# Kernel optimization log

Measured on AMD Instinct MI355X. Metric: run time of the kernel, lower is better.

The kernel has to match this reference:

```python
import jax, jax.numpy as jnp
import numpy as np

N, E = 50000, 800000
IN, HID, OUT = 256, 128, 64


def setup_inputs() -> dict:
    key = jax.random.key(0)
    ks = jax.random.split(key, 8)
    x = jax.random.normal(ks[0], (N, IN), dtype=jnp.float32)
    edge_index = jax.random.randint(ks[1], (2, E), 0, N, dtype=jnp.int64)
    # PyG GCNConv: Linear weight [out, in] (glorot-ish), bias [out] (zeros init; use small randn for a nontrivial baseline)
    W1 = jax.random.normal(ks[2], (HID, IN), dtype=jnp.float32) / np.sqrt(IN)
    b1 = jax.random.normal(ks[3], (HID,), dtype=jnp.float32) * 0.01
    Wmu = jax.random.normal(ks[4], (OUT, HID), dtype=jnp.float32) / np.sqrt(HID)
    bmu = jax.random.normal(ks[5], (OUT,), dtype=jnp.float32) * 0.01
    Wlv = jax.random.normal(ks[6], (OUT, HID), dtype=jnp.float32) / np.sqrt(HID)
    blv = jax.random.normal(ks[7], (OUT,), dtype=jnp.float32) * 0.01
    return {"x": x, "edge_index": edge_index, "W1": W1, "b1": b1,
            "Wmu": Wmu, "bmu": bmu, "Wlv": Wlv, "blv": blv}


def reference(x, edge_index, W1, b1, Wmu, bmu, Wlv, blv):
    n = x.shape[0]
    loop = jnp.arange(n, dtype=edge_index.dtype)
    src = jnp.concatenate([edge_index[0], loop])  # [E+N]
    dst = jnp.concatenate([edge_index[1], loop])
    # symmetric normalization with self-loops: deg computed on destinations
    deg = jax.ops.segment_sum(jnp.ones_like(dst, dtype=x.dtype), dst, num_segments=n)
    dis = jax.lax.rsqrt(deg)  # deg >= 1 due to self-loops
    norm = dis[src] * dis[dst]  # [E+N]

    def gcn(h, W, b):
        hw = h @ W.T                                   # [N, out]
        msg = hw[src] * norm[:, None]                  # [E+N, out] gather + scale
        return jax.ops.segment_sum(msg, dst, num_segments=n) + b

    h = jax.nn.relu(gcn(x, W1, b1))
    # dropout(p=0.5) is identity in eval mode
    return (gcn(h, Wmu, bmu), gcn(h, Wlv, blv))
```

## Files before the change

### kernel.cpp

```cpp
#include <hip/hip_runtime.h>

#define N_NODES 50000
#define N_EDGES 800000
#define DIN 256
#define DHID 128
#define DOUT 64
#define NB_SCAN 49
#define SENT N_NODES

typedef __attribute__((ext_vector_type(8))) short short8;
typedef __attribute__((ext_vector_type(4))) float f32x4;

static __device__ __forceinline__ short f2bf(float f) {
    union { float f; unsigned u; } v; v.f = f;
    unsigned r = v.u + 0x7FFFu + ((v.u >> 16) & 1u);
    return (short)(r >> 16);
}
static __device__ __forceinline__ float bflo(unsigned p) {
    union { unsigned u; float f; } v; v.u = p << 16; return v.f;
}
static __device__ __forceinline__ float bfhi(unsigned p) {
    union { unsigned u; float f; } v; v.u = p & 0xFFFF0000u; return v.f;
}


__global__ void count_kernel(const int* __restrict__ ei, int* __restrict__ cnt,
                             int* __restrict__ loc) {
    int stride = gridDim.x * blockDim.x;
    for (int e = blockIdx.x * blockDim.x + threadIdx.x; e < N_EDGES; e += stride) {
        loc[e] = atomicAdd(&cnt[ei[N_EDGES + e]], 1);
    }
}

__global__ __launch_bounds__(1024) void bsum_kernel(const int* __restrict__ cnt,
                                                    int* __restrict__ bsum) {
    __shared__ int ws[16];
    int tid = threadIdx.x, i = blockIdx.x * 1024 + tid;
    int v = (i < N_NODES) ? cnt[i] : 0;
    v = (v + 7) & ~7;
    #pragma unroll
    for (int off = 32; off >= 1; off >>= 1) v += __shfl_xor(v, off);
    if ((tid & 63) == 0) ws[tid >> 6] = v;
    __syncthreads();
    if (tid == 0) {
        int s = 0;
        #pragma unroll
        for (int w = 0; w < 16; ++w) s += ws[w];
        bsum[blockIdx.x] = s;
    }
}

__global__ void bscan_kernel(const int* __restrict__ bsum, int* __restrict__ bo,
                             int* __restrict__ rowptr) {
    int l = threadIdx.x;
    int v = (l < NB_SCAN) ? bsum[l] : 0;
    int x = v;
    #pragma unroll
    for (int off = 1; off < 64; off <<= 1) {
        int y = __shfl_up(x, off);
        if (l >= off) x += y;
    }
    if (l < NB_SCAN) bo[l] = x - v;
    if (l == 63) rowptr[N_NODES] = x;
}

__global__ __launch_bounds__(1024) void scan_apply_kernel(const int* __restrict__ cnt,
        const int* __restrict__ bo, int* __restrict__ rowptr,
        float* __restrict__ dis, int* __restrict__ col) {
    __shared__ int wsum[16];
    int tid = threadIdx.x, i = blockIdx.x * 1024 + tid;
    int lane = tid & 63, wid = tid >> 6;
    int v = (i < N_NODES) ? cnt[i] : 0;
    int p = (v + 7) & ~7;
    int x = p;
    #pragma unroll
    for (int off = 1; off < 64; off <<= 1) {
        int y = __shfl_up(x, off);
        if (lane >= off) x += y;
    }
    if (lane == 63) wsum[wid] = x;
    __syncthreads();
    if (tid == 0) {
        int s = 0;
        #pragma unroll
        for (int w = 0; w < 16; ++w) { int t = wsum[w]; wsum[w] = s; s += t; }
    }
    __syncthreads();
    int excl = bo[blockIdx.x] + wsum[wid] + (x - p);
    if (i < N_NODES) {
        rowptr[i] = excl;
        dis[i] = rsqrtf((float)(v + 1));
        for (int q = v; q < p; ++q) col[excl + q] = SENT;
    }
}

__global__ void fill_kernel(const int* __restrict__ ei, const int* __restrict__ loc,
                            const int* __restrict__ rowptr, int* __restrict__ col) {
    int stride = gridDim.x * blockDim.x;
    for (int e = blockIdx.x * blockDim.x + threadIdx.x; e < N_EDGES; e += stride) {
        int s = ei[e];
        int d = ei[N_EDGES + e];
        col[rowptr[d] + loc[e]] = s;
    }
}


__global__ void wprep_kernel(const float* __restrict__ W1, const float* __restrict__ Wmu,
                             const float* __restrict__ Wlv, short* __restrict__ W1b,
                             short* __restrict__ Wctb) {
    int tid = blockIdx.x * blockDim.x + threadIdx.x;
    if (tid < DHID * DIN) {
        W1b[tid] = f2bf(W1[tid]);
    } else if (tid < DHID * DIN + 2 * DOUT * DHID) {
        int t = tid - DHID * DIN;
        Wctb[t] = f2bf((t < DOUT * DHID) ? Wmu[t] : Wlv[t - DOUT * DHID]);
    }
}


__global__ __launch_bounds__(256) void gemm1_mfma_kernel(const float* __restrict__ x,
        const short* __restrict__ W1b, const float* __restrict__ dis,
        short* __restrict__ u1b) {
    const int lane = threadIdx.x & 63, w = threadIdx.x >> 6;
    const int l15 = lane & 15, kg = lane >> 4;
    const int nb = blockIdx.x * 64;
    const int r0 = nb + w * 16 + l15;
    const bool valid = r0 < N_NODES;
    const float* xrow = x + (size_t)r0 * DIN;

    float4 f0[8], f1[8];
    #pragma unroll
    for (int ks = 0; ks < 8; ++ks) {
        const int k0 = ks * 32 + kg * 8;
        if (valid) {
            f0[ks] = *(const float4*)(xrow + k0);
            f1[ks] = *(const float4*)(xrow + k0 + 4);
        } else {
            f0[ks] = float4{0.f, 0.f, 0.f, 0.f};
            f1[ks] = float4{0.f, 0.f, 0.f, 0.f};
        }
    }
    short8 a[8];
    #pragma unroll
    for (int ks = 0; ks < 8; ++ks) {
        a[ks][0] = f2bf(f0[ks].x); a[ks][1] = f2bf(f0[ks].y);
        a[ks][2] = f2bf(f0[ks].z); a[ks][3] = f2bf(f0[ks].w);
        a[ks][4] = f2bf(f1[ks].x); a[ks][5] = f2bf(f1[ks].y);
        a[ks][6] = f2bf(f1[ks].z); a[ks][7] = f2bf(f1[ks].w);
    }

    f32x4 acc[8] = {};
    #pragma unroll
    for (int ks = 0; ks < 8; ++ks) {
        const int k0 = ks * 32 + kg * 8;
        #pragma unroll
        for (int c = 0; c < 8; ++c) {
            short8 b = *(const short8*)(W1b + (size_t)(c * 16 + l15) * DIN + k0);
            acc[c] = __builtin_amdgcn_mfma_f32_16x16x32_bf16(a[ks], b, acc[c], 0, 0, 0);
        }
    }

    const int rb = nb + w * 16 + kg * 4;
    float dv[4];
    #pragma unroll
    for (int e = 0; e < 4; ++e) dv[e] = (rb + e < N_NODES) ? dis[rb + e] : 0.f;
    #pragma unroll
    for (int c = 0; c < 8; ++c) {
        #pragma unroll
        for (int e = 0; e < 4; ++e) {
            int r = rb + e;
            if (r < N_NODES)
                u1b[(size_t)r * DHID + c * 16 + l15] = f2bf(acc[c][e] * dv[e]);
        }
    }
}


template <bool LAYER1>
__global__ __launch_bounds__(256) void pull_kernel(const int* __restrict__ rowptr,
        const int* __restrict__ col, const short* __restrict__ uin,
        const float* __restrict__ dis, const float* __restrict__ b1,
        unsigned* __restrict__ uout) {
    const int wid = threadIdx.x >> 6, lane = threadIdx.x & 63;
    const int i = blockIdx.x * 4 + wid;
    if (i >= N_NODES) return;
    const int beg = rowptr[i], end = rowptr[i + 1];
    const unsigned* __restrict__ up = (const unsigned*)uin;
    float ax = 0.f, ay = 0.f;
    for (int base = beg; base < end; base += 64) {
        const int rem = end - base;
        const int m = rem < 64 ? rem : 64;
        int cv = (lane < m) ? col[base + lane] : SENT;
        for (int t = 0; t < m; t += 8) {
            int c0 = __shfl(cv, t);
            int c1 = __shfl(cv, t + 1);
            int c2 = __shfl(cv, t + 2);
            int c3 = __shfl(cv, t + 3);
            int c4 = __shfl(cv, t + 4);
            int c5 = __shfl(cv, t + 5);
            int c6 = __shfl(cv, t + 6);
            int c7 = __shfl(cv, t + 7);
            unsigned v0 = up[(size_t)c0 * 64 + lane];
            unsigned v1 = up[(size_t)c1 * 64 + lane];
            unsigned v2 = up[(size_t)c2 * 64 + lane];
            unsigned v3 = up[(size_t)c3 * 64 + lane];
            unsigned v4 = up[(size_t)c4 * 64 + lane];
            unsigned v5 = up[(size_t)c5 * 64 + lane];
            unsigned v6 = up[(size_t)c6 * 64 + lane];
            unsigned v7 = up[(size_t)c7 * 64 + lane];
            ax += bflo(v0); ay += bfhi(v0);
            ax += bflo(v1); ay += bfhi(v1);
            ax += bflo(v2); ay += bfhi(v2);
            ax += bflo(v3); ay += bfhi(v3);
            ax += bflo(v4); ay += bfhi(v4);
            ax += bflo(v5); ay += bfhi(v5);
            ax += bflo(v6); ay += bfhi(v6);
            ax += bflo(v7); ay += bfhi(v7);
        }
    }
    const float di = dis[i];
    const unsigned sv = up[(size_t)i * 64 + lane];
    float tx = di * (ax + bflo(sv));
    float ty = di * (ay + bfhi(sv));
    if (LAYER1) {
        float2 b = *(const float2*)(b1 + lane * 2);
        tx = fmaxf(tx + b.x, 0.f) * di;
        ty = fmaxf(ty + b.y, 0.f) * di;
    }
    unsigned o = ((unsigned)(unsigned short)f2bf(tx)) |
                 (((unsigned)(unsigned short)f2bf(ty)) << 16);
    uout[(size_t)i * 64 + lane] = o;
}


__global__ __launch_bounds__(256) void gemm2_mfma_kernel(const short* __restrict__ a2b,
        const short* __restrict__ Wctb, const float* __restrict__ bmu,
        const float* __restrict__ blv, float* __restrict__ out) {
    const int lane = threadIdx.x & 63, w = threadIdx.x >> 6;
    const int l15 = lane & 15, kg = lane >> 4;
    const int nb = blockIdx.x * 64;
    const int r0 = nb + w * 16 + l15;
    const bool valid = r0 < N_NODES;
    const short* arow = a2b + (size_t)r0 * DHID;

    f32x4 acc[8] = {};
    #pragma unroll
    for (int ks = 0; ks < 4; ++ks) {
        const int k0 = ks * 32 + kg * 8;
        short8 a = valid ? *(const short8*)(arow + k0)
                         : short8{0, 0, 0, 0, 0, 0, 0, 0};
        #pragma unroll
        for (int c = 0; c < 8; ++c) {
            short8 b = *(const short8*)(Wctb + (size_t)(c * 16 + l15) * DHID + k0);
            acc[c] = __builtin_amdgcn_mfma_f32_16x16x32_bf16(a, b, acc[c], 0, 0, 0);
        }
    }

    float bias[8];
    #pragma unroll
    for (int c = 0; c < 8; ++c) {
        int j = c * 16 + l15;
        bias[c] = (j < DOUT) ? bmu[j] : blv[j - DOUT];
    }
    const int rb = nb + w * 16 + kg * 4;
    #pragma unroll
    for (int c = 0; c < 8; ++c) {
        const int j = c * 16 + l15;
        float* dst = (j < DOUT) ? (out + j)
                                : (out + (size_t)N_NODES * DOUT + (j - DOUT));
        #pragma unroll
        for (int e = 0; e < 4; ++e) {
            int r = rb + e;
            if (r < N_NODES)
                dst[(size_t)r * DOUT] = acc[c][e] + bias[c];
        }
    }
}


extern "C" void kernel_launch(void* const* d_in, const int* in_sizes, int n_in,
                              void* d_out, int out_size, void* d_ws, size_t ws_size,
                              hipStream_t stream) {
    const float* x   = (const float*)d_in[0];
    const int*   ei  = (const int*)d_in[1];
    const float* W1  = (const float*)d_in[2];
    const float* b1  = (const float*)d_in[3];
    const float* Wmu = (const float*)d_in[4];
    const float* bmu = (const float*)d_in[5];
    const float* Wlv = (const float*)d_in[6];
    const float* blv = (const float*)d_in[7];
    float* out = (float*)d_out;

    char* ws = (char*)d_ws;
    size_t off = 0;
    auto alloc = [&](size_t bytes) -> char* {
        char* p = ws + off;
        off += (bytes + 255) & ~(size_t)255;
        return p;
    };
    const size_t COL_CAP = (size_t)N_EDGES + 8 * (size_t)N_NODES + 64;
    int*   cnt    = (int*)  alloc((size_t)N_NODES * 4);
    int*   rowptr = (int*)  alloc((size_t)(N_NODES + 1) * 4);
    float* dis    = (float*)alloc((size_t)N_NODES * 4);
    int*   loc    = (int*)  alloc((size_t)N_EDGES * 4);
    int*   col    = (int*)  alloc(COL_CAP * 4);
    int*   bsum   = (int*)  alloc((size_t)NB_SCAN * 4);
    int*   bo     = (int*)  alloc((size_t)NB_SCAN * 4);
    short* W1b    = (short*)alloc((size_t)DHID * DIN * 2);
    short* Wctb   = (short*)alloc((size_t)2 * DOUT * DHID * 2);
    short* u1b    = (short*)alloc((size_t)(N_NODES + 1) * DHID * 2);
    short* u2b    = (short*)alloc((size_t)(N_NODES + 1) * DHID * 2);
    short* a2b    = (short*)alloc((size_t)N_NODES * DHID * 2);

    hipMemsetAsync(cnt, 0, (size_t)N_NODES * 4, stream);
    hipMemsetAsync(u1b + (size_t)N_NODES * DHID, 0, DHID * 2, stream);
    hipMemsetAsync(u2b + (size_t)N_NODES * DHID, 0, DHID * 2, stream);
    wprep_kernel<<<192, 256, 0, stream>>>(W1, Wmu, Wlv, W1b, Wctb);
    count_kernel<<<1024, 256, 0, stream>>>(ei, cnt, loc);
    bsum_kernel<<<NB_SCAN, 1024, 0, stream>>>(cnt, bsum);
    bscan_kernel<<<1, 64, 0, stream>>>(bsum, bo, rowptr);
    scan_apply_kernel<<<NB_SCAN, 1024, 0, stream>>>(cnt, bo, rowptr, dis, col);
    fill_kernel<<<1024, 256, 0, stream>>>(ei, loc, rowptr, col);
    gemm1_mfma_kernel<<<(N_NODES + 63) / 64, 256, 0, stream>>>(x, W1b, dis, u1b);
    pull_kernel<true><<<N_NODES / 4, 256, 0, stream>>>(rowptr, col, u1b, dis, b1,
                                                       (unsigned*)u2b);
    pull_kernel<false><<<N_NODES / 4, 256, 0, stream>>>(rowptr, col, u2b, dis, nullptr,
                                                        (unsigned*)a2b);
    gemm2_mfma_kernel<<<(N_NODES + 63) / 64, 256, 0, stream>>>(a2b, Wctb, bmu, blv, out);
}
```

Measured before the change: 281.9 us.

## Split fp32-to-bf16 conversion of x into a separate prep kernel before GEMM1

Adds an xprep kernel that scales x rows by dis and converts them to bf16 in a separate buffer. GEMM1 then reads bf16 directly, and its work is split so each wave computes 16 rows by 64 columns, with 32 rows per block. The aim is to lower register pressure in the GEMM and give it more blocks. The cost is an extra full pass over x: a 51 MB fp32 read and a 25 MB bf16 write plus read back. It also reuses u1b as a2b to save workspace.

```diff
diff --git a/kernel.cpp b/kernel.cpp
--- a/kernel.cpp
+++ b/kernel.cpp
@@ -118,59 +118,59 @@
 }
 
 
-__global__ __launch_bounds__(256) void gemm1_mfma_kernel(const float* __restrict__ x,
-        const short* __restrict__ W1b, const float* __restrict__ dis,
-        short* __restrict__ u1b) {
+__global__ __launch_bounds__(256) void xprep_kernel(const float* __restrict__ x,
+        const float* __restrict__ dis, short* __restrict__ xb) {
+    const int total = N_NODES * (DIN / 8);
+    int stride = gridDim.x * blockDim.x;
+    for (int c = blockIdx.x * blockDim.x + threadIdx.x; c < total; c += stride) {
+        int row = c >> 5;
+        float d = dis[row];
+        const float* src = x + (size_t)c * 8;
+        float4 f0 = *(const float4*)src;
+        float4 f1 = *(const float4*)(src + 4);
+        short8 o;
+        o[0] = f2bf(f0.x * d); o[1] = f2bf(f0.y * d);
+        o[2] = f2bf(f0.z * d); o[3] = f2bf(f0.w * d);
+        o[4] = f2bf(f1.x * d); o[5] = f2bf(f1.y * d);
+        o[6] = f2bf(f1.z * d); o[7] = f2bf(f1.w * d);
+        *(short8*)(xb + (size_t)c * 8) = o;
+    }
+}
+
+
+__global__ __launch_bounds__(256) void gemm1_mfma_kernel(const short* __restrict__ xb,
+        const short* __restrict__ W1b, short* __restrict__ u1b) {
     const int lane = threadIdx.x & 63, w = threadIdx.x >> 6;
     const int l15 = lane & 15, kg = lane >> 4;
-    const int nb = blockIdx.x * 64;
-    const int r0 = nb + w * 16 + l15;
+    const int rowg = w >> 1, colh = w & 1;
+    const int nb = blockIdx.x * 32 + rowg * 16;
+    const int r0 = nb + l15;
     const bool valid = r0 < N_NODES;
-    const float* xrow = x + (size_t)r0 * DIN;
-
-    float4 f0[8], f1[8];
+    const short* arow = xb + (size_t)r0 * DIN;
+
+    f32x4 acc[4] = {};
     #pragma unroll
     for (int ks = 0; ks < 8; ++ks) {
         const int k0 = ks * 32 + kg * 8;
-        if (valid) {
-            f0[ks] = *(const float4*)(xrow + k0);
-            f1[ks] = *(const float4*)(xrow + k0 + 4);
-        } else {
-            f0[ks] = float4{0.f, 0.f, 0.f, 0.f};
-            f1[ks] = float4{0.f, 0.f, 0.f, 0.f};
-        }
-    }
-    short8 a[8];
-    #pragma unroll
-    for (int ks = 0; ks < 8; ++ks) {
-        a[ks][0] = f2bf(f0[ks].x); a[ks][1] = f2bf(f0[ks].y);
-        a[ks][2] = f2bf(f0[ks].z); a[ks][3] = f2bf(f0[ks].w);
-        a[ks][4] = f2bf(f1[ks].x); a[ks][5] = f2bf(f1[ks].y);
-        a[ks][6] = f2bf(f1[ks].z); a[ks][7] = f2bf(f1[ks].w);
-    }
-
-    f32x4 acc[8] = {};
-    #pragma unroll
-    for (int ks = 0; ks < 8; ++ks) {
-        const int k0 = ks * 32 + kg * 8;
-        #pragma unroll
-        for (int c = 0; c < 8; ++c) {
-            short8 b = *(const short8*)(W1b + (size_t)(c * 16 + l15) * DIN + k0);
-            acc[c] = __builtin_amdgcn_mfma_f32_16x16x32_bf16(a[ks], b, acc[c], 0, 0, 0);
-        }
-    }
-
-    const int rb = nb + w * 16 + kg * 4;
-    float dv[4];
-    #pragma unroll
-    for (int e = 0; e < 4; ++e) dv[e] = (rb + e < N_NODES) ? dis[rb + e] : 0.f;
-    #pragma unroll
-    for (int c = 0; c < 8; ++c) {
+        short8 a = valid ? *(const short8*)(arow + k0)
+                         : short8{0, 0, 0, 0, 0, 0, 0, 0};
+        #pragma unroll
+        for (int c = 0; c < 4; ++c) {
+            const int cc = colh * 4 + c;
+            short8 b = *(const short8*)(W1b + (size_t)(cc * 16 + l15) * DIN + k0);
+            acc[c] = __builtin_amdgcn_mfma_f32_16x16x32_bf16(a, b, acc[c], 0, 0, 0);
+        }
+    }
+
+    const int rb = nb + kg * 4;
+    #pragma unroll
+    for (int c = 0; c < 4; ++c) {
+        const int j = (colh * 4 + c) * 16 + l15;
         #pragma unroll
         for (int e = 0; e < 4; ++e) {
             int r = rb + e;
             if (r < N_NODES)
-                u1b[(size_t)r * DHID + c * 16 + l15] = f2bf(acc[c][e] * dv[e]);
+                u1b[(size_t)r * DHID + j] = f2bf(acc[c][e]);
         }
     }
 }
@@ -308,9 +308,10 @@
     int*   bo     = (int*)  alloc((size_t)NB_SCAN * 4);
     short* W1b    = (short*)alloc((size_t)DHID * DIN * 2);
     short* Wctb   = (short*)alloc((size_t)2 * DOUT * DHID * 2);
+    short* xb     = (short*)alloc((size_t)N_NODES * DIN * 2);
     short* u1b    = (short*)alloc((size_t)(N_NODES + 1) * DHID * 2);
     short* u2b    = (short*)alloc((size_t)(N_NODES + 1) * DHID * 2);
-    short* a2b    = (short*)alloc((size_t)N_NODES * DHID * 2);
+    short* a2b    = u1b;
 
     hipMemsetAsync(cnt, 0, (size_t)N_NODES * 4, stream);
     hipMemsetAsync(u1b + (size_t)N_NODES * DHID, 0, DHID * 2, stream);
@@ -321,7 +322,8 @@
     bscan_kernel<<<1, 64, 0, stream>>>(bsum, bo, rowptr);
     scan_apply_kernel<<<NB_SCAN, 1024, 0, stream>>>(cnt, bo, rowptr, dis, col);
     fill_kernel<<<1024, 256, 0, stream>>>(ei, loc, rowptr, col);
-    gemm1_mfma_kernel<<<(N_NODES + 63) / 64, 256, 0, stream>>>(x, W1b, dis, u1b);
+    xprep_kernel<<<2048, 256, 0, stream>>>(x, dis, xb);
+    gemm1_mfma_kernel<<<(N_NODES + 31) / 32, 256, 0, stream>>>(xb, W1b, u1b);
     pull_kernel<true><<<N_NODES / 4, 256, 0, stream>>>(rowptr, col, u1b, dis, b1,
                                                        (unsigned*)u2b);
     pull_kernel<false><<<N_NODES / 4, 256, 0, stream>>>(rowptr, col, u2b, dis, nullptr,
```

New measurement: 284.0 us. No clear change (+0.7%).
